# Optimization experiments

Measured on AMD Instinct MI355X. Metric: run time of the kernel, lower is better.

The kernel has to match this reference:

```python
import jax, jax.numpy as jnp
import numpy as np

DIM = 1024
HEADS = 16
HEAD_DIM = DIM // HEADS

def setup_inputs() -> dict:
    key = jax.random.key(0)
    ks = jax.random.split(key, 6)
    s = 0.02
    return {
        "x": jax.random.normal(ks[0], (2, 2048, DIM), dtype=jnp.float32),
        "w_qkv": jax.random.normal(ks[1], (DIM, 3 * DIM), dtype=jnp.float32) * s,
        "w_proj": jax.random.normal(ks[2], (DIM, DIM), dtype=jnp.float32) * s,
        "b_proj": jnp.zeros((DIM,), dtype=jnp.float32),
        "ln_gamma": jnp.ones((DIM,), dtype=jnp.float32),
        "ln_beta": jnp.zeros((DIM,), dtype=jnp.float32),
    }

def layer_norm(x, gamma, beta, eps=1e-5):
    mu = jnp.mean(x, axis=-1, keepdims=True)
    var = jnp.var(x, axis=-1, keepdims=True)
    return (x - mu) * jax.lax.rsqrt(var + eps) * gamma + beta

def reference(x, w_qkv, w_proj, b_proj, ln_gamma, ln_beta):
    B, N, C = x.shape
    residual = x
    h = layer_norm(x, ln_gamma, ln_beta)
    qkv = h @ w_qkv  # [B,N,3C]
    qkv = qkv.reshape(B, N, 3, HEADS, HEAD_DIM)
    q = jnp.transpose(qkv[:, :, 0], (0, 2, 1, 3))  # [B,H,N,D]
    k = jnp.transpose(qkv[:, :, 1], (0, 2, 1, 3))
    v = jnp.transpose(qkv[:, :, 2], (0, 2, 1, 3))
    scale = 1.0 / jnp.sqrt(jnp.float32(HEAD_DIM))
    attn = jnp.einsum('bhqd,bhkd->bhqk', q, k) * scale
    attn = jax.nn.softmax(attn, axis=-1)
    out = jnp.einsum('bhqk,bhkd->bhqd', attn, v)  # [B,H,N,D]
    out = jnp.transpose(out, (0, 2, 1, 3)).reshape(B, N, C)
    out = out @ w_proj + b_proj
    return out + residual
```

## Files before the change

kernel.cpp:

```cpp
#include <hip/hip_runtime.h>

#define DIM   1024
#define HEADS 16
#define HDIM  64
#define BATCH 2
#define SEQ   2048
#define TOK   (BATCH*SEQ)
#define MEG   1048576

typedef __bf16 bf16x8 __attribute__((ext_vector_type(8)));
typedef float  f32x4  __attribute__((ext_vector_type(4)));
typedef float  f32x16 __attribute__((ext_vector_type(16)));

__device__ __forceinline__ float b2f(ushort u) {
    union { unsigned int u32; float f; } x; x.u32 = ((unsigned int)u) << 16; return x.f;
}
__device__ __forceinline__ ushort f2b(float f) {
    union { float f; unsigned int u32; } x; x.f = f;
    unsigned int r = x.u32 + 0x7FFFu + ((x.u32 >> 16) & 1u);
    return (ushort)(r >> 16);
}
__device__ __forceinline__ void gload_lds16(const ushort* g, void* l) {
    __builtin_amdgcn_global_load_lds((const __attribute__((address_space(1))) void*)g,
                                     (__attribute__((address_space(3))) void*)l, 16, 0, 0);
}
__device__ __forceinline__ float fexp2(float x) {
    float r; asm("v_exp_f32 %0, %1" : "=v"(r) : "v"(x)); return r;
}
__device__ __forceinline__ unsigned int cvtpk_bf16(float lo, float hi) {
    unsigned int r; asm("v_cvt_pk_bf16_f32 %0, %1, %2" : "=v"(r) : "v"(lo), "v"(hi)); return r;
}
__device__ __forceinline__ void plane32swap(unsigned int &a, unsigned int &b) {
    asm("v_permlane32_swap_b32 %0, %1" : "+v"(a), "+v"(b));
}

__global__ void transpose_f2b_k(const float* __restrict__ src, ushort* __restrict__ dst,
                                int R, int Cc) {
    __shared__ ushort tile[32][33];
    int c0 = blockIdx.x * 32, r0 = blockIdx.y * 32;
    int tx = threadIdx.x, ty = threadIdx.y;
#pragma unroll
    for (int i = 0; i < 4; i++)
        tile[ty + 8 * i][tx] = f2b(src[(long)(r0 + ty + 8 * i) * Cc + c0 + tx]);
    __syncthreads();
#pragma unroll
    for (int i = 0; i < 4; i++)
        dst[(long)(c0 + ty + 8 * i) * R + r0 + tx] = tile[tx][ty + 8 * i];
}

__global__ __launch_bounds__(256)
void ln_k(const float* __restrict__ x, const float* __restrict__ gamma,
          const float* __restrict__ beta, ushort* __restrict__ h) {
    __shared__ float red[8];
    int row = blockIdx.x, tid = threadIdx.x;
    const float* xr = x + (long)row * DIM;
    float4 xv = *(const float4*)(xr + tid * 4);
    float s1 = xv.x + xv.y + xv.z + xv.w;
    float s2 = xv.x * xv.x + xv.y * xv.y + xv.z * xv.z + xv.w * xv.w;
#pragma unroll
    for (int off = 32; off; off >>= 1) {
        s1 += __shfl_down(s1, off);
        s2 += __shfl_down(s2, off);
    }
    int wid = tid >> 6, lane = tid & 63;
    if (lane == 0) { red[wid * 2] = s1; red[wid * 2 + 1] = s2; }
    __syncthreads();
    s1 = red[0] + red[2] + red[4] + red[6];
    s2 = red[1] + red[3] + red[5] + red[7];
    float mu  = s1 * (1.0f / DIM);
    float var = s2 * (1.0f / DIM) - mu * mu;
    float rs  = rsqrtf(var + 1e-5f);
    float4 gv = *(const float4*)(gamma + tid * 4);
    float4 bv = *(const float4*)(beta + tid * 4);
    ushort4 ov;
    ov.x = f2b((xv.x - mu) * rs * gv.x + bv.x);
    ov.y = f2b((xv.y - mu) * rs * gv.y + bv.y);
    ov.z = f2b((xv.z - mu) * rs * gv.z + bv.z);
    ov.w = f2b((xv.w - mu) * rs * gv.w + bv.w);
    *(ushort4*)(h + (long)row * DIM + tid * 4) = ov;
}

__global__ __launch_bounds__(256, 3)
void gemm_qkv_k(const ushort* __restrict__ A, const ushort* __restrict__ Bt,
                ushort* __restrict__ qp, ushort* __restrict__ kp, ushort* __restrict__ vp) {
    __shared__ ushort smem[16384];
    int tid  = threadIdx.x;
    int wid  = tid >> 6, lane = tid & 63;
    int quad = lane >> 4, l16 = lane & 15;
    int wm = wid >> 1, wn = wid & 1;
    int rowbase = blockIdx.y * 128;
    int colbase = blockIdx.x * 128;

    f32x4 acc[4][4];
#pragma unroll
    for (int i = 0; i < 4; i++)
#pragma unroll
        for (int j = 0; j < 4; j++) acc[i][j] = (f32x4){0.f, 0.f, 0.f, 0.f};

    for (int k0 = 0; k0 < DIM; k0 += 64) {
#pragma unroll
        for (int p = 0; p < 2; p++) {
            int c = wid * 2 + p;
            int r = c * 16 + (lane >> 2);
            int ac = (lane & 3) * 8;
#pragma unroll
            for (int pnl = 0; pnl < 2; pnl++) {
                int cc = k0 + pnl * 32 + ac;
                gload_lds16(A  + (long)(rowbase + r) * DIM + cc,
                            &smem[pnl * 4096 + c * 16 * 32]);
                gload_lds16(Bt + (long)(colbase + r) * DIM + cc,
                            &smem[8192 + pnl * 4096 + c * 16 * 32]);
            }
        }
        __syncthreads();
#pragma unroll
        for (int pnl = 0; pnl < 2; pnl++) {
            bf16x8 fa[4], fb[4];
#pragma unroll
            for (int t = 0; t < 4; t++)
                fa[t] = *(const bf16x8*)(&smem[pnl * 4096 + (wm * 64 + t * 16 + l16) * 32 + quad * 8]);
#pragma unroll
            for (int t = 0; t < 4; t++)
                fb[t] = *(const bf16x8*)(&smem[8192 + pnl * 4096 + (wn * 64 + t * 16 + l16) * 32 + quad * 8]);
#pragma unroll
            for (int i = 0; i < 4; i++)
#pragma unroll
                for (int j = 0; j < 4; j++)
                    acc[i][j] = __builtin_amdgcn_mfma_f32_16x16x32_bf16(fa[i], fb[j], acc[i][j], 0, 0, 0);
        }
        __syncthreads();
    }

    if (colbase >= 2048) {
#pragma unroll
        for (int i = 0; i < 4; i++)
#pragma unroll
            for (int j = 0; j < 4; j++) {
                int cl = wn * 64 + j * 16 + l16;
                int rl = wm * 64 + i * 16 + quad * 4;
#pragma unroll
                for (int r = 0; r < 4; r++)
                    smem[cl * 128 + rl + r] = f2b(acc[i][j][r]);
            }
        __syncthreads();
        int b = rowbase >> 11, nnb = rowbase & 2047;
        int hbase = (colbase - 2048) >> 6;
#pragma unroll
        for (int i = 0; i < 8; i++) {
            int id = i * 256 + tid;
            int cl = id >> 4;
            int off = (id & 15) * 8;
            int hh = hbase + (cl >> 6), d = cl & 63;
            uint4 val = *(const uint4*)(&smem[cl * 128 + off]);
            *(uint4*)(vp + (((long)b * HEADS + hh) * HDIM + d) * SEQ + nnb + off) = val;
        }
    } else {
#pragma unroll
        for (int i = 0; i < 4; i++)
#pragma unroll
            for (int j = 0; j < 4; j++) {
                int m0  = rowbase + wm * 64 + i * 16 + quad * 4;
                int col = colbase + wn * 64 + j * 16 + l16;
                int part = col >> 10, rem = col & 1023;
                int head = rem >> 6, d = rem & 63;
                ushort* dst = (part == 0) ? qp : kp;
#pragma unroll
                for (int r = 0; r < 4; r++) {
                    float v = acc[i][j][r];
                    int mm = m0 + r;
                    int b = mm >> 11, nn = mm & 2047;
                    float sv = (part == 0) ? v * 0.18033688011f : v;
                    dst[((((long)b * HEADS + head) * SEQ + nn) << 6) + d] = f2b(sv);
                }
            }
    }
}

__global__ __launch_bounds__(256, 3)
void gemm_proj_k(const ushort* __restrict__ A, const ushort* __restrict__ Bt,
                 const float* __restrict__ bias, const float* __restrict__ xres,
                 float* __restrict__ outp) {
    __shared__ ushort As[2][128][32];
    __shared__ ushort Bs[2][64][32];
    int tid  = threadIdx.x;
    int wid  = tid >> 6, lane = tid & 63;
    int quad = lane >> 4, l16 = lane & 15;
    int rowbase = blockIdx.y * 128;
    int colbase = blockIdx.x * 64;
    int arow = lane >> 2, acol = (lane & 3) * 8;

    f32x4 acc[2][4];
#pragma unroll
    for (int i = 0; i < 2; i++)
#pragma unroll
        for (int j = 0; j < 4; j++) acc[i][j] = (f32x4){0.f, 0.f, 0.f, 0.f};

    for (int k0 = 0; k0 < DIM; k0 += 64) {
#pragma unroll
        for (int p = 0; p < 2; p++) {
            int c = wid * 2 + p;
            int r = c * 16 + arow;
            int mm = rowbase + r;
            int bq = mm >> 11, nn = mm & 2047;
#pragma unroll
            for (int pnl = 0; pnl < 2; pnl++) {
                int cc = k0 + pnl * 32 + acol;
                int head = cc >> 6, d = cc & 63;
                gload_lds16(A + ((((long)bq * HEADS + head) * SEQ + nn) << 6) + d,
                            &As[pnl][c * 16][0]);
            }
        }
        {
            int r = wid * 16 + arow;
#pragma unroll
            for (int pnl = 0; pnl < 2; pnl++) {
                int cc = k0 + pnl * 32 + acol;
                gload_lds16(Bt + (long)(colbase + r) * DIM + cc, &Bs[pnl][wid * 16][0]);
            }
        }
        __syncthreads();
#pragma unroll
        for (int pnl = 0; pnl < 2; pnl++) {
            bf16x8 fa[2], fb[4];
#pragma unroll
            for (int t = 0; t < 2; t++)
                fa[t] = *(const bf16x8*)(&As[pnl][wid * 32 + t * 16 + l16][quad * 8]);
#pragma unroll
            for (int t = 0; t < 4; t++)
                fb[t] = *(const bf16x8*)(&Bs[pnl][t * 16 + l16][quad * 8]);
#pragma unroll
            for (int i = 0; i < 2; i++)
#pragma unroll
                for (int j = 0; j < 4; j++)
                    acc[i][j] = __builtin_amdgcn_mfma_f32_16x16x32_bf16(fa[i], fb[j], acc[i][j], 0, 0, 0);
        }
        __syncthreads();
    }

#pragma unroll
    for (int i = 0; i < 2; i++)
#pragma unroll
        for (int j = 0; j < 4; j++) {
            int m0  = rowbase + wid * 32 + i * 16 + quad * 4;
            int col = colbase + j * 16 + l16;
#pragma unroll
            for (int r = 0; r < 4; r++) {
                int mm = m0 + r;
                outp[(long)mm * DIM + col] = acc[i][j][r] + bias[col] + xres[(long)mm * DIM + col];
            }
        }
}

__global__ __launch_bounds__(256, 4)
void attn_k(ushort* qio, const ushort* __restrict__ kg,
            const ushort* __restrict__ vt) {
    __shared__ __align__(16) ushort Kp[2][2048];
    __shared__ __align__(16) ushort Vs[2][2048];
    int bh = blockIdx.y;
    int tid = threadIdx.x, wid = tid >> 6, lane = tid & 63;
    int l31 = lane & 31, hi = lane >> 5;
    ushort* qh = qio + (long)bh * SEQ * HDIM;
    const ushort* kh = kg + (long)bh * SEQ * HDIM;
    const ushort* vh = vt + (long)bh * HDIM * SEQ;

    int kr = tid & 31, kc = tid >> 5;
    int kofs = kr * 64 + ((kc ^ (kr & 7)) * 8);
    int vrow = tid & 63;
    int vslot = ((tid >> 6) + (vrow >> 1)) & 3;
    int vgc = (vslot ^ (vrow & 3)) * 8;
    int vofs = vrow * 32 + vslot * 8;

    int qrow0 = blockIdx.x * 128 + wid * 32;
    bf16x8 qf[4];
#pragma unroll
    for (int ks = 0; ks < 4; ks++)
        qf[ks] = *(const bf16x8*)(qh + (long)(qrow0 + l31) * HDIM + ks * 16 + hi * 8);

    f32x16 o0 = {}, o1 = {};
    f32x4 lac = {0.f, 0.f, 0.f, 0.f};

    uint4 kreg = *(const uint4*)(kh + (long)kr * HDIM + kc * 8);
    uint4 vreg = *(const uint4*)(vh + (long)vrow * SEQ + vgc);
    *(uint4*)(&Kp[0][kofs]) = kreg;
    *(uint4*)(&Vs[0][vofs]) = vreg;

    const int NIT = SEQ / 32;
    for (int it = 0; it < NIT; ++it) {
        int buf = it & 1;
        if (it + 1 < NIT) {
            int kt = (it + 1) * 32;
            kreg = *(const uint4*)(kh + (long)(kt + kr) * HDIM + kc * 8);
            vreg = *(const uint4*)(vh + (long)vrow * SEQ + kt + vgc);
        }
        __syncthreads();

        f32x16 sc = {};
        __builtin_amdgcn_s_setprio(1);
#pragma unroll
        for (int ks = 0; ks < 4; ks++) {
            bf16x8 kb = *(const bf16x8*)(
                &Kp[buf][l31 * 64 + (((2 * ks + hi) ^ (l31 & 7)) * 8)]);
            sc = __builtin_amdgcn_mfma_f32_32x32x16_bf16(kb, qf[ks], sc, 0, 0, 0);
        }
        __builtin_amdgcn_s_setprio(0);

        float e[16];
#pragma unroll
        for (int r = 0; r < 16; r++) e[r] = fexp2(sc[r]);
#pragma unroll
        for (int r = 0; r < 4; r++)
            lac += (f32x4){e[4 * r], e[4 * r + 1], e[4 * r + 2], e[4 * r + 3]};

        unsigned int pk0 = cvtpk_bf16(e[0], e[1]),   pk1 = cvtpk_bf16(e[2], e[3]);
        unsigned int pk2 = cvtpk_bf16(e[4], e[5]),   pk3 = cvtpk_bf16(e[6], e[7]);
        unsigned int pk4 = cvtpk_bf16(e[8], e[9]),   pk5 = cvtpk_bf16(e[10], e[11]);
        unsigned int pk6 = cvtpk_bf16(e[12], e[13]), pk7 = cvtpk_bf16(e[14], e[15]);
        plane32swap(pk0, pk2);
        plane32swap(pk1, pk3);
        plane32swap(pk4, pk6);
        plane32swap(pk5, pk7);
        union { unsigned int u[4]; bf16x8 v; } pa0, pa1;
        pa0.u[0] = pk0; pa0.u[1] = pk1; pa0.u[2] = pk2; pa0.u[3] = pk3;
        pa1.u[0] = pk4; pa1.u[1] = pk5; pa1.u[2] = pk6; pa1.u[3] = pk7;

        __builtin_amdgcn_s_setprio(1);
        {
            int d0 = l31;
            bf16x8 v00 = *(const bf16x8*)(&Vs[buf][d0 * 32 + ((hi ^ (d0 & 3)) * 8)]);
            bf16x8 v01 = *(const bf16x8*)(&Vs[buf][d0 * 32 + (((2 + hi) ^ (d0 & 3)) * 8)]);
            o0 = __builtin_amdgcn_mfma_f32_32x32x16_bf16(pa0.v, v00, o0, 0, 0, 0);
            o0 = __builtin_amdgcn_mfma_f32_32x32x16_bf16(pa1.v, v01, o0, 0, 0, 0);
            int d1 = 32 + l31;
            bf16x8 v10 = *(const bf16x8*)(&Vs[buf][d1 * 32 + ((hi ^ (d1 & 3)) * 8)]);
            bf16x8 v11 = *(const bf16x8*)(&Vs[buf][d1 * 32 + (((2 + hi) ^ (d1 & 3)) * 8)]);
            o1 = __builtin_amdgcn_mfma_f32_32x32x16_bf16(pa0.v, v10, o1, 0, 0, 0);
            o1 = __builtin_amdgcn_mfma_f32_32x32x16_bf16(pa1.v, v11, o1, 0, 0, 0);
        }
        __builtin_amdgcn_s_setprio(0);

        if (it + 1 < NIT) {
            *(uint4*)(&Kp[buf ^ 1][kofs]) = kreg;
            *(uint4*)(&Vs[buf ^ 1][vofs]) = vreg;
        }
    }

    float t = lac[0] + lac[1] + lac[2] + lac[3];
    t += __shfl_xor(t, 32);
    float linv = 1.0f / t;
#pragma unroll
    for (int r = 0; r < 16; r++) {
        int qrow = (r & 3) + 8 * (r >> 2) + 4 * hi;
        float lr = __shfl(linv, qrow);
        long ro = (long)(qrow0 + qrow) * HDIM;
        qh[ro + l31]      = f2b(o0[r] * lr);
        qh[ro + 32 + l31] = f2b(o1[r] * lr);
    }
}

extern "C" void kernel_launch(void* const* d_in, const int* in_sizes, int n_in,
                              void* d_out, int out_size, void* d_ws, size_t ws_size,
                              hipStream_t stream) {
    const float* x      = (const float*)d_in[0];
    const float* w_qkv  = (const float*)d_in[1];
    const float* w_proj = (const float*)d_in[2];
    const float* b_proj = (const float*)d_in[3];
    const float* gamma  = (const float*)d_in[4];
    const float* beta   = (const float*)d_in[5];
    float* out = (float*)d_out;

    ushort* ws   = (ushort*)d_ws;
    ushort* h    = ws;
    ushort* wqt  = ws + (size_t)4 * MEG;
    ushort* qb   = ws + (size_t)7 * MEG;
    ushort* kb   = ws + (size_t)11 * MEG;
    ushort* vtb  = ws + (size_t)15 * MEG;

    transpose_f2b_k<<<dim3(3 * DIM / 32, DIM / 32), dim3(32, 8), 0, stream>>>(
        w_qkv, wqt, DIM, 3 * DIM);
    ln_k<<<dim3(TOK), dim3(256), 0, stream>>>(x, gamma, beta, h);
    gemm_qkv_k<<<dim3(3 * DIM / 128, TOK / 128), dim3(256), 0, stream>>>(
        h, wqt, qb, kb, vtb);
    attn_k<<<dim3(SEQ / 128, BATCH * HEADS), dim3(256), 0, stream>>>(qb, kb, vtb);
    transpose_f2b_k<<<dim3(DIM / 32, DIM / 32), dim3(32, 8), 0, stream>>>(
        w_proj, kb, DIM, DIM);
    gemm_proj_k<<<dim3(DIM / 64, TOK / 128), dim3(256), 0, stream>>>(
        qb, kb, b_proj, x, out);
}
```

Measured before the change: 183.3 us.

## Double attention KV tile to 64 keys per iteration with unified swizzled LDS layout

The attention kernel now processes 64 keys per iteration instead of 32, issuing two QK MFMAs per k-step and four PV k-groups. This halves the number of block barriers and loop iterations and gives more independent MFMA work per sync. K and V staging share one XOR-swizzled 64-wide layout with two 16-byte loads each per thread. LDS per block doubles and launch bounds drop to 2 blocks per CU, so occupancy may fall and register pressure rises.

```diff
diff --git a/kernel.cpp b/kernel.cpp
--- a/kernel.cpp
+++ b/kernel.cpp
@@ -32,6 +32,15 @@
 }
 __device__ __forceinline__ void plane32swap(unsigned int &a, unsigned int &b) {
     asm("v_permlane32_swap_b32 %0, %1" : "+v"(a), "+v"(b));
+}
+__device__ __forceinline__ bf16x8 pack8(float e0, float e1, float e2, float e3,
+                                        float e4, float e5, float e6, float e7) {
+    unsigned int a = cvtpk_bf16(e0, e1), b = cvtpk_bf16(e2, e3);
+    unsigned int c = cvtpk_bf16(e4, e5), d = cvtpk_bf16(e6, e7);
+    plane32swap(a, c); plane32swap(b, d);
+    union { unsigned int u[4]; bf16x8 v; } r;
+    r.u[0] = a; r.u[1] = b; r.u[2] = c; r.u[3] = d;
+    return r.v;
 }
 
 __global__ void transpose_f2b_k(const float* __restrict__ src, ushort* __restrict__ dst,
@@ -251,24 +260,23 @@
         }
 }
 
-__global__ __launch_bounds__(256, 4)
+__global__ __launch_bounds__(256, 2)
 void attn_k(ushort* qio, const ushort* __restrict__ kg,
             const ushort* __restrict__ vt) {
-    __shared__ __align__(16) ushort Kp[2][2048];
-    __shared__ __align__(16) ushort Vs[2][2048];
+    __shared__ __align__(16) ushort Kp[2][4096];
+    __shared__ __align__(16) ushort Vs[2][4096];
     int bh = blockIdx.y;
-    int tid = threadIdx.x, wid = tid >> 6, lane = tid & 63;
+    int tid = threadIdx.x, wid = tid >> 6;
+    int lane = tid & 63;
     int l31 = lane & 31, hi = lane >> 5;
     ushort* qh = qio + (long)bh * SEQ * HDIM;
     const ushort* kh = kg + (long)bh * SEQ * HDIM;
     const ushort* vh = vt + (long)bh * HDIM * SEQ;
 
-    int kr = tid & 31, kc = tid >> 5;
-    int kofs = kr * 64 + ((kc ^ (kr & 7)) * 8);
-    int vrow = tid & 63;
-    int vslot = ((tid >> 6) + (vrow >> 1)) & 3;
-    int vgc = (vslot ^ (vrow & 3)) * 8;
-    int vofs = vrow * 32 + vslot * 8;
+    int srow = tid >> 3, schk = tid & 7;
+    int sofs = srow * 64 + ((schk ^ (srow & 7)) * 8);
+    const ushort* kbase = kh + (long)srow * HDIM + schk * 8;
+    const ushort* vbase = vh + (long)srow * SEQ + schk * 8;
 
     int qrow0 = blockIdx.x * 128 + wid * 32;
     bf16x8 qf[4];
@@ -279,68 +287,69 @@
     f32x16 o0 = {}, o1 = {};
     f32x4 lac = {0.f, 0.f, 0.f, 0.f};
 
-    uint4 kreg = *(const uint4*)(kh + (long)kr * HDIM + kc * 8);
-    uint4 vreg = *(const uint4*)(vh + (long)vrow * SEQ + vgc);
-    *(uint4*)(&Kp[0][kofs]) = kreg;
-    *(uint4*)(&Vs[0][vofs]) = vreg;
-
-    const int NIT = SEQ / 32;
+    uint4 kr0 = *(const uint4*)(kbase);
+    uint4 kr1 = *(const uint4*)(kbase + 32 * HDIM);
+    uint4 vr0 = *(const uint4*)(vbase);
+    uint4 vr1 = *(const uint4*)(vbase + 32 * SEQ);
+    *(uint4*)(&Kp[0][sofs])        = kr0;
+    *(uint4*)(&Kp[0][sofs + 2048]) = kr1;
+    *(uint4*)(&Vs[0][sofs])        = vr0;
+    *(uint4*)(&Vs[0][sofs + 2048]) = vr1;
+
+    const int NIT = SEQ / 64;
     for (int it = 0; it < NIT; ++it) {
         int buf = it & 1;
         if (it + 1 < NIT) {
-            int kt = (it + 1) * 32;
-            kreg = *(const uint4*)(kh + (long)(kt + kr) * HDIM + kc * 8);
-            vreg = *(const uint4*)(vh + (long)vrow * SEQ + kt + vgc);
-        }
-        __syncthreads();
-
-        f32x16 sc = {};
+            int kt = (it + 1) * 64;
+            kr0 = *(const uint4*)(kbase + (long)kt * HDIM);
+            kr1 = *(const uint4*)(kbase + (long)(kt + 32) * HDIM);
+            vr0 = *(const uint4*)(vbase + kt);
+            vr1 = *(const uint4*)(vbase + 32 * SEQ + kt);
+        }
+        __syncthreads();
+
+        f32x16 sc0 = {}, sc1 = {};
         __builtin_amdgcn_s_setprio(1);
 #pragma unroll
         for (int ks = 0; ks < 4; ks++) {
-            bf16x8 kb = *(const bf16x8*)(
-                &Kp[buf][l31 * 64 + (((2 * ks + hi) ^ (l31 & 7)) * 8)]);
-            sc = __builtin_amdgcn_mfma_f32_32x32x16_bf16(kb, qf[ks], sc, 0, 0, 0);
+            int psl = ((2 * ks + hi) ^ (l31 & 7)) * 8;
+            bf16x8 ka = *(const bf16x8*)(&Kp[buf][l31 * 64 + psl]);
+            bf16x8 kb = *(const bf16x8*)(&Kp[buf][(32 + l31) * 64 + psl]);
+            sc0 = __builtin_amdgcn_mfma_f32_32x32x16_bf16(ka, qf[ks], sc0, 0, 0, 0);
+            sc1 = __builtin_amdgcn_mfma_f32_32x32x16_bf16(kb, qf[ks], sc1, 0, 0, 0);
         }
         __builtin_amdgcn_s_setprio(0);
 
-        float e[16];
-#pragma unroll
-        for (int r = 0; r < 16; r++) e[r] = fexp2(sc[r]);
+        float e0[16], e1[16];
+#pragma unroll
+        for (int r = 0; r < 16; r++) { e0[r] = fexp2(sc0[r]); e1[r] = fexp2(sc1[r]); }
 #pragma unroll
         for (int r = 0; r < 4; r++)
-            lac += (f32x4){e[4 * r], e[4 * r + 1], e[4 * r + 2], e[4 * r + 3]};
-
-        unsigned int pk0 = cvtpk_bf16(e[0], e[1]),   pk1 = cvtpk_bf16(e[2], e[3]);
-        unsigned int pk2 = cvtpk_bf16(e[4], e[5]),   pk3 = cvtpk_bf16(e[6], e[7]);
-        unsigned int pk4 = cvtpk_bf16(e[8], e[9]),   pk5 = cvtpk_bf16(e[10], e[11]);
-        unsigned int pk6 = cvtpk_bf16(e[12], e[13]), pk7 = cvtpk_bf16(e[14], e[15]);
-        plane32swap(pk0, pk2);
-        plane32swap(pk1, pk3);
-        plane32swap(pk4, pk6);
-        plane32swap(pk5, pk7);
-        union { unsigned int u[4]; bf16x8 v; } pa0, pa1;
-        pa0.u[0] = pk0; pa0.u[1] = pk1; pa0.u[2] = pk2; pa0.u[3] = pk3;
-        pa1.u[0] = pk4; pa1.u[1] = pk5; pa1.u[2] = pk6; pa1.u[3] = pk7;
+            lac += (f32x4){e0[4*r], e0[4*r+1], e0[4*r+2], e0[4*r+3]}
+                 + (f32x4){e1[4*r], e1[4*r+1], e1[4*r+2], e1[4*r+3]};
+
+        bf16x8 pa0 = pack8(e0[0], e0[1], e0[2],  e0[3],  e0[4],  e0[5],  e0[6],  e0[7]);
+        bf16x8 pa1 = pack8(e0[8], e0[9], e0[10], e0[11], e0[12], e0[13], e0[14], e0[15]);
+        bf16x8 pa2 = pack8(e1[0], e1[1], e1[2],  e1[3],  e1[4],  e1[5],  e1[6],  e1[7]);
+        bf16x8 pa3 = pack8(e1[8], e1[9], e1[10], e1[11], e1[12], e1[13], e1[14], e1[15]);
 
         __builtin_amdgcn_s_setprio(1);
-        {
-            int d0 = l31;
-            bf16x8 v00 = *(const bf16x8*)(&Vs[buf][d0 * 32 + ((hi ^ (d0 & 3)) * 8)]);
-            bf16x8 v01 = *(const bf16x8*)(&Vs[buf][d0 * 32 + (((2 + hi) ^ (d0 & 3)) * 8)]);
-            o0 = __builtin_amdgcn_mfma_f32_32x32x16_bf16(pa0.v, v00, o0, 0, 0, 0);
-            o0 = __builtin_amdgcn_mfma_f32_32x32x16_bf16(pa1.v, v01, o0, 0, 0, 0);
-            int d1 = 32 + l31;
-            bf16x8 v10 = *(const bf16x8*)(&Vs[buf][d1 * 32 + ((hi ^ (d1 & 3)) * 8)]);
-            bf16x8 v11 = *(const bf16x8*)(&Vs[buf][d1 * 32 + (((2 + hi) ^ (d1 & 3)) * 8)]);
-            o1 = __builtin_amdgcn_mfma_f32_32x32x16_bf16(pa0.v, v10, o1, 0, 0, 0);
-            o1 = __builtin_amdgcn_mfma_f32_32x32x16_bf16(pa1.v, v11, o1, 0, 0, 0);
+#pragma unroll
+        for (int g = 0; g < 4; g++) {
+            int psl = ((2 * g + hi) ^ (l31 & 7)) * 8;
+            bf16x8 v0 = *(const bf16x8*)(&Vs[buf][l31 * 64 + psl]);
+            bf16x8 v1 = *(const bf16x8*)(&Vs[buf][(32 + l31) * 64 + psl]);
+            bf16x8 pg = (g == 0) ? pa0 : (g == 1) ? pa1 : (g == 2) ? pa2 : pa3;
+            o0 = __builtin_amdgcn_mfma_f32_32x32x16_bf16(pg, v0, o0, 0, 0, 0);
+            o1 = __builtin_amdgcn_mfma_f32_32x32x16_bf16(pg, v1, o1, 0, 0, 0);
         }
         __builtin_amdgcn_s_setprio(0);
 
         if (it + 1 < NIT) {
-            *(uint4*)(&Kp[buf ^ 1][kofs]) = kreg;
-            *(uint4*)(&Vs[buf ^ 1][vofs]) = vreg;
+            *(uint4*)(&Kp[buf ^ 1][sofs])        = kr0;
+            *(uint4*)(&Kp[buf ^ 1][sofs + 2048]) = kr1;
+            *(uint4*)(&Vs[buf ^ 1][sofs])        = vr0;
+            *(uint4*)(&Vs[buf ^ 1][sofs + 2048]) = vr1;
         }
     }
 
```

Result: no change. 184.3 us (+0.6%).
